# Optimization experiments

Hardware: AMD Instinct MI355X
Metric: run time of the kernel (lower is better)

## Reference

```python
import jax, jax.numpy as jnp
import numpy as np
import math

L, D_T, D, NL, NH, FFN, C, B = 24, 1024, 256, 12, 4, 1024, 2, 2048
HD = D // NH


def _layernorm(x, g, b, eps=1e-5):
    m = jnp.mean(x, axis=-1, keepdims=True)
    v = jnp.mean(jnp.square(x - m), axis=-1, keepdims=True)
    return (x - m) * jax.lax.rsqrt(v + eps) * g + b


def _rotate_half(x):
    x1, x2 = jnp.split(x, 2, axis=-1)
    return jnp.concatenate([-x2, x1], axis=-1)


def setup_inputs() -> dict:
    key = jax.random.key(0)
    ks = iter(jax.random.split(key, 64))
    n = lambda shape, s=0.02: jax.random.normal(next(ks), shape, dtype=jnp.float32) * s
    inp = {}
    inp['teacher_cls'] = jax.random.normal(next(ks), (B, L, D_T), dtype=jnp.float32)
    # input LN + projection
    inp['in_ln_g'] = jnp.ones((D_T,), jnp.float32); inp['in_ln_b'] = jnp.zeros((D_T,), jnp.float32)
    inp['proj_w'] = n((D, D_T)); inp['proj_b'] = jnp.zeros((D,), jnp.float32)
    # RoPE caches (buffers)
    inv_freq = 1.0 / (10000.0 ** (np.arange(0, D, 2, dtype=np.float32) / D))
    t = np.arange(L, dtype=np.float32)
    freqs = np.einsum('i,j->ij', t, inv_freq)
    emb = np.concatenate([freqs, freqs], axis=-1)
    inp['cos_cached'] = jnp.asarray(np.cos(emb)[None])  # [1,L,D]
    inp['sin_cached'] = jnp.asarray(np.sin(emb)[None])
    inp['pre_ln_g'] = jnp.ones((D,), jnp.float32); inp['pre_ln_b'] = jnp.zeros((D,), jnp.float32)
    # stacked transformer layer params [NL, ...]
    inp['l_ln1_g'] = jnp.ones((NL, D), jnp.float32); inp['l_ln1_b'] = jnp.zeros((NL, D), jnp.float32)
    inp['l_inw'] = n((NL, 3 * D, D)); inp['l_inb'] = jnp.zeros((NL, 3 * D), jnp.float32)
    inp['l_outw'] = n((NL, D, D)); inp['l_outb'] = jnp.zeros((NL, D), jnp.float32)
    inp['l_ln2_g'] = jnp.ones((NL, D), jnp.float32); inp['l_ln2_b'] = jnp.zeros((NL, D), jnp.float32)
    inp['l_w12'] = n((NL, 2 * FFN, D)); inp['l_b12'] = jnp.zeros((NL, 2 * FFN), jnp.float32)
    inp['l_w3'] = n((NL, D, FFN)); inp['l_b3'] = jnp.zeros((NL, D), jnp.float32)
    inp['post_ln_g'] = jnp.ones((D,), jnp.float32); inp['post_ln_b'] = jnp.zeros((D,), jnp.float32)
    # entropy gate
    inp['eg_w1'] = n((L, D, 8), 0.01); inp['eg_b1'] = jnp.zeros((L, 8), jnp.float32)
    inp['eg_w2'] = n((L, 8, 1), 0.01); inp['eg_b2'] = jnp.zeros((L, 1), jnp.float32)
    # per-position heads (stacked)
    inp['halt_w'] = n((L, D + 1)); inp['halt_b'] = jnp.full((L,), -4.0, jnp.float32)
    inp['cls_w'] = n((L, C, D)); inp['cls_b'] = jnp.zeros((L, C), jnp.float32)
    return inp


def _mha(x, inw, inb, outw, outb, mask):
    Bb, Ll, Dd = x.shape
    qkv = x @ inw.T + inb                              # [B,L,3D]
    q, k, v = jnp.split(qkv, 3, axis=-1)
    def heads(t):
        return t.reshape(Bb, Ll, NH, HD).transpose(0, 2, 1, 3)  # [B,H,L,hd]
    q, k, v = heads(q), heads(k), heads(v)
    scores = jnp.einsum('bhqd,bhkd->bhqk', q, k) / math.sqrt(HD)
    scores = jnp.where(mask, -jnp.inf, scores)
    attn = jax.nn.softmax(scores, axis=-1)
    o = jnp.einsum('bhqk,bhkd->bhqd', attn, v)
    o = o.transpose(0, 2, 1, 3).reshape(Bb, Ll, Dd)
    return o @ outw.T + outb


def reference(teacher_cls, in_ln_g, in_ln_b, proj_w, proj_b, cos_cached, sin_cached,
              pre_ln_g, pre_ln_b, l_ln1_g, l_ln1_b, l_inw, l_inb, l_outw, l_outb,
              l_ln2_g, l_ln2_b, l_w12, l_b12, l_w3, l_b3, post_ln_g, post_ln_b,
              eg_w1, eg_b1, eg_w2, eg_b2, halt_w, halt_b, cls_w, cls_b):
    x = _layernorm(teacher_cls, in_ln_g, in_ln_b)
    x = x @ proj_w.T + proj_b                          # [B,L,D]
    x = x * cos_cached + _rotate_half(x) * sin_cached  # RoPE
    z = _layernorm(x, pre_ln_g, pre_ln_b)
    mask = jnp.triu(jnp.ones((L, L), bool), 1)         # causal
    for i in range(NL):
        xn = _layernorm(z, l_ln1_g[i], l_ln1_b[i])
        z = z + _mha(xn, l_inw[i], l_inb[i], l_outw[i], l_outb[i], mask)
        xn = _layernorm(z, l_ln2_g[i], l_ln2_b[i])
        w12_out = xn @ l_w12[i].T + l_b12[i]           # [B,L,2*FFN]
        x1, x2 = jnp.split(w12_out, 2, axis=-1)
        hidden = jax.nn.silu(x1) * x2
        z = z + hidden @ l_w3[i].T + l_b3[i]
    z = _layernorm(z, post_ln_g, post_ln_b)
    # batched per-position classifier heads
    class_logits = jnp.einsum('bld,lcd->blc', z, cls_w) + cls_b   # [B,L,C]
    log_probs = jax.nn.log_softmax(class_logits, axis=-1)
    probs = jnp.exp(log_probs)
    probs_safe = jnp.clip(probs, 1e-10, 1.0)
    ent = -jnp.sum(probs_safe * jnp.log(probs_safe), axis=-1, keepdims=True)
    ent_norm = jnp.clip(ent / math.log(C), 0.0, 1.0)              # [B,L,1]
    # entropy gate
    h = jnp.tanh(jnp.einsum('bld,ldh->blh', z, eg_w1) + eg_b1)
    gate = jax.nn.sigmoid(jnp.einsum('blh,lho->blo', h, eg_w2) + eg_b2)
    gated = ent_norm * gate                                        # [B,L,1]
    # batched per-position halting heads
    combined = jnp.concatenate([z, gated], axis=-1)                # [B,L,D+1]
    halting_logits = jnp.einsum('bld,ld->bl', combined, halt_w) + halt_b
    return (halting_logits, class_logits, z)
```

## Files before the change

kernel.cpp:

```cpp
#include <hip/hip_runtime.h>
#include <hip/hip_bf16.h>
#include <math.h>

#define L_SEQ 24
#define DT 1024
#define DM 256
#define NLAYER 12
#define NHEAD 4
#define HDIM 64
#define FFND 1024
#define NCLS 2
#define NBATCH 2048
#define NTOK (NBATCH*L_SEQ)

typedef float f32x4 __attribute__((ext_vector_type(4)));
typedef __bf16 bf16x4 __attribute__((ext_vector_type(4)));
typedef __bf16 bf16x8 __attribute__((ext_vector_type(8)));

#define GLDS16(gp, lp) __builtin_amdgcn_global_load_lds((const __attribute__((address_space(1))) void*)(gp), (__attribute__((address_space(3))) void*)(lp), 16, 0, 0)
#define VMWAIT(N) asm volatile("s_waitcnt vmcnt(" #N ")" ::: "memory")
#define LGKM0()   asm volatile("s_waitcnt lgkmcnt(0)" ::: "memory")

__device__ inline float wred_sum(float v){
#pragma unroll
  for (int o = 32; o > 0; o >>= 1) v += __shfl_xor(v, o);
  return v;
}
__device__ inline float wred_max(float v){
#pragma unroll
  for (int o = 32; o > 0; o >>= 1) v = fmaxf(v, __shfl_xor(v, o));
  return v;
}

__device__ __forceinline__ void stage16x32(const __bf16* __restrict__ g, int ldk, int k0,
                                           __bf16* ldsbase, int lane, int rowbase){
  int r = rowbase + (lane >> 2);
  int cs = (lane & 3) ^ ((lane >> 3) & 3);
  GLDS16(g + (size_t)r*ldk + k0 + cs*8, ldsbase);
}
__device__ __forceinline__ bf16x8 frag32(const __bf16* tile, int row, int lane){
  int p = (lane >> 4) ^ ((row >> 1) & 3);
  return *(const bf16x8*)(tile + (row << 5) + (p << 3));
}

__device__ __forceinline__ int xcd_work(){
  int nwg = gridDim.x, bid = blockIdx.x;
  return (bid & 7) * (nwg >> 3) + (bid >> 3);
}

__global__ void cvt_bf16_kernel(const float* __restrict__ in, __bf16* __restrict__ out, int n4){
  int i = blockIdx.x * blockDim.x + threadIdx.x;
  int stride = gridDim.x * blockDim.x;
  for (; i < n4; i += stride){
    float4 v = ((const float4*)in)[i];
    bf16x4 o;
    o[0] = (__bf16)v.x; o[1] = (__bf16)v.y; o[2] = (__bf16)v.z; o[3] = (__bf16)v.w;
    ((bf16x4*)out)[i] = o;
  }
}

__global__ __launch_bounds__(256) void ln1024_kernel(
    const float* __restrict__ in, const float* __restrict__ g, const float* __restrict__ bb,
    __bf16* __restrict__ out){
  int row = blockIdx.x;
  int tid = threadIdx.x, wid = tid >> 6, lane = tid & 63;
  float4 x = ((const float4*)(in + (size_t)row*DT))[tid];
  float s = x.x + x.y + x.z + x.w;
  float q = x.x*x.x + x.y*x.y + x.z*x.z + x.w*x.w;
  s = wred_sum(s); q = wred_sum(q);
  __shared__ float red[8];
  if (lane == 0){ red[wid] = s; red[4+wid] = q; }
  __syncthreads();
  s = red[0]+red[1]+red[2]+red[3];
  q = red[4]+red[5]+red[6]+red[7];
  float mean = s * (1.f/DT);
  float rstd = rsqrtf(q*(1.f/DT) - mean*mean + 1e-5f);
  float4 gv = ((const float4*)g)[tid], bv = ((const float4*)bb)[tid];
  bf16x4 o;
  o[0] = (__bf16)((x.x-mean)*rstd*gv.x + bv.x);
  o[1] = (__bf16)((x.y-mean)*rstd*gv.y + bv.y);
  o[2] = (__bf16)((x.z-mean)*rstd*gv.z + bv.z);
  o[3] = (__bf16)((x.w-mean)*rstd*gv.w + bv.w);
  ((bf16x4*)(out + (size_t)row*DT))[tid] = o;
}

__global__ __launch_bounds__(256) void rope_preln_kernel(
    float* __restrict__ z, const float* __restrict__ cosc, const float* __restrict__ sinc,
    const float* __restrict__ g, const float* __restrict__ bb,
    const float* __restrict__ g1, const float* __restrict__ b1, __bf16* __restrict__ xnb){
  int row = blockIdx.x*4 + (threadIdx.x >> 6);
  int lane = threadIdx.x & 63;
  int l = row % L_SEQ;
  float4 x = ((const float4*)(z + (size_t)row*DM))[lane];
  float4 p;
  p.x = __shfl_xor(x.x, 32); p.y = __shfl_xor(x.y, 32);
  p.z = __shfl_xor(x.z, 32); p.w = __shfl_xor(x.w, 32);
  float sgn = (lane < 32) ? -1.f : 1.f;
  float4 c = ((const float4*)(cosc + l*DM))[lane];
  float4 sn = ((const float4*)(sinc + l*DM))[lane];
  float4 xr;
  xr.x = x.x*c.x + sgn*p.x*sn.x;
  xr.y = x.y*c.y + sgn*p.y*sn.y;
  xr.z = x.z*c.z + sgn*p.z*sn.z;
  xr.w = x.w*c.w + sgn*p.w*sn.w;
  float s = wred_sum(xr.x + xr.y + xr.z + xr.w);
  float q = wred_sum(xr.x*xr.x + xr.y*xr.y + xr.z*xr.z + xr.w*xr.w);
  float mean = s * (1.f/DM);
  float rstd = rsqrtf(q*(1.f/DM) - mean*mean + 1e-5f);
  float4 gv = ((const float4*)g)[lane], bv = ((const float4*)bb)[lane];
  float4 y;
  y.x = (xr.x-mean)*rstd*gv.x + bv.x;
  y.y = (xr.y-mean)*rstd*gv.y + bv.y;
  y.z = (xr.z-mean)*rstd*gv.z + bv.z;
  y.w = (xr.w-mean)*rstd*gv.w + bv.w;
  ((float4*)(z + (size_t)row*DM))[lane] = y;
  float s2 = wred_sum(y.x + y.y + y.z + y.w);
  float q2 = wred_sum(y.x*y.x + y.y*y.y + y.z*y.z + y.w*y.w);
  float mean2 = s2 * (1.f/DM);
  float rstd2 = rsqrtf(q2*(1.f/DM) - mean2*mean2 + 1e-5f);
  float4 g1v = ((const float4*)g1)[lane], b1v = ((const float4*)b1)[lane];
  bf16x4 o;
  o[0] = (__bf16)((y.x-mean2)*rstd2*g1v.x + b1v.x);
  o[1] = (__bf16)((y.y-mean2)*rstd2*g1v.y + b1v.y);
  o[2] = (__bf16)((y.z-mean2)*rstd2*g1v.z + b1v.z);
  o[3] = (__bf16)((y.w-mean2)*rstd2*g1v.w + b1v.w);
  ((bf16x4*)(xnb + (size_t)row*DM))[lane] = o;
}

template<int MODE, int K>
__global__ __launch_bounds__(256) void gemm128_kernel(
    const __bf16* __restrict__ A, const __bf16* __restrict__ W,
    const float* __restrict__ bias,
    float* __restrict__ Cf, __bf16* __restrict__ Cb,
    int N, int nt){
  __shared__ __align__(16) __bf16 As[2][128*32];
  __shared__ __align__(16) __bf16 Bs[2][128*32];
  int work = xcd_work();
  int bm = work / nt, bn = work % nt;
  int wid = threadIdx.x >> 6, lane = threadIdx.x & 63;
  int wr = wid >> 1, wc = wid & 1;
  int li = lane & 15, g4 = (lane >> 4) << 2;
  f32x4 acc[4][4] = {};
  const __bf16* ga = A + (size_t)bm*128*K;
  const __bf16* gb = W + (size_t)bn*128*K;
  const int NT = K/32;
  auto STAGE = [&](int b, int t){
    int k0 = t*32;
    stage16x32(ga, K, k0, &As[b][(wid*32)<<5],      lane, wid*32);
    stage16x32(ga, K, k0, &As[b][(wid*32+16)<<5],   lane, wid*32+16);
    stage16x32(gb, K, k0, &Bs[b][(wid*32)<<5],      lane, wid*32);
    stage16x32(gb, K, k0, &Bs[b][(wid*32+16)<<5],   lane, wid*32+16);
  };
  STAGE(0, 0);
  STAGE(1, 1);
  int cur = 0;
  for (int t = 0; t < NT; t++){
    if (t + 1 < NT) { VMWAIT(4); } else { VMWAIT(0); }
    __builtin_amdgcn_s_barrier();
    bf16x8 xf[4], wf[4];
#pragma unroll
    for (int mi = 0; mi < 4; mi++) xf[mi] = frag32(As[cur], wr*64 + mi*16 + li, lane);
#pragma unroll
    for (int ni = 0; ni < 4; ni++) wf[ni] = frag32(Bs[cur], wc*64 + ni*16 + li, lane);
    LGKM0();
    __builtin_amdgcn_sched_barrier(0);
    __builtin_amdgcn_s_barrier();
    if (t + 2 < NT) STAGE(cur, t+2);
    __builtin_amdgcn_s_setprio(1);
#pragma unroll
    for (int ni = 0; ni < 4; ni++)
#pragma unroll
      for (int mi = 0; mi < 4; mi++)
        acc[ni][mi] = __builtin_amdgcn_mfma_f32_16x16x32_bf16(wf[ni], xf[mi], acc[ni][mi], 0, 0, 0);
    __builtin_amdgcn_s_setprio(0);
    cur ^= 1;
  }
#pragma unroll
  for (int mi = 0; mi < 4; mi++){
    int m = bm*128 + wr*64 + mi*16 + li;
#pragma unroll
    for (int ni = 0; ni < 4; ni++){
      int n = bn*128 + wc*64 + ni*16 + g4;
      f32x4 bv = *(const f32x4*)(bias + n);
      f32x4 o = acc[ni][mi] + bv;
      if (MODE == 0){
        *(f32x4*)(Cf + (size_t)m*N + n) = o;
      } else {
        bf16x4 ob;
        ob[0] = (__bf16)o[0]; ob[1] = (__bf16)o[1]; ob[2] = (__bf16)o[2]; ob[3] = (__bf16)o[3];
        *(bf16x4*)(Cb + (size_t)m*N + n) = ob;
      }
    }
  }
}

__global__ __launch_bounds__(256) void gemm_glu_kernel(
    const __bf16* __restrict__ A, const __bf16* __restrict__ W12,
    const float* __restrict__ bias, __bf16* __restrict__ H){
  __shared__ __align__(16) __bf16 As[2][128*32];
  __shared__ __align__(16) __bf16 B1s[2][128*32];
  __shared__ __align__(16) __bf16 B2s[2][128*32];
  const int K = 256;
  int work = xcd_work();
  int bm = work >> 3, bn = work & 7;
  int wid = threadIdx.x >> 6, lane = threadIdx.x & 63;
  int wr = wid >> 1, wc = wid & 1;
  int li = lane & 15, g4 = (lane >> 4) << 2;
  f32x4 acc1[4][4] = {}, acc2[4][4] = {};
  const __bf16* ga  = A   + (size_t)bm*128*K;
  const __bf16* gb1 = W12 + (size_t)bn*128*K;
  const __bf16* gb2 = gb1 + (size_t)1024*K;
  auto STAGE = [&](int b, int t){
    int k0 = t*32;
    stage16x32(ga,  K, k0, &As[b][(wid*32)<<5],     lane, wid*32);
    stage16x32(ga,  K, k0, &As[b][(wid*32+16)<<5],  lane, wid*32+16);
    stage16x32(gb1, K, k0, &B1s[b][(wid*32)<<5],    lane, wid*32);
    stage16x32(gb1, K, k0, &B1s[b][(wid*32+16)<<5], lane, wid*32+16);
    stage16x32(gb2, K, k0, &B2s[b][(wid*32)<<5],    lane, wid*32);
    stage16x32(gb2, K, k0, &B2s[b][(wid*32+16)<<5], lane, wid*32+16);
  };
  STAGE(0, 0);
  STAGE(1, 1);
  int cur = 0;
  for (int t = 0; t < 8; t++){
    if (t + 1 < 8) { VMWAIT(6); } else { VMWAIT(0); }
    __builtin_amdgcn_s_barrier();
    bf16x8 xf[4], w1f[4], w2f[4];
#pragma unroll
    for (int mi = 0; mi < 4; mi++) xf[mi] = frag32(As[cur], wr*64 + mi*16 + li, lane);
#pragma unroll
    for (int ni = 0; ni < 4; ni++){
      w1f[ni] = frag32(B1s[cur], wc*64 + ni*16 + li, lane);
      w2f[ni] = frag32(B2s[cur], wc*64 + ni*16 + li, lane);
    }
    LGKM0();
    __builtin_amdgcn_sched_barrier(0);
    __builtin_amdgcn_s_barrier();
    if (t + 2 < 8) STAGE(cur, t+2);
    __builtin_amdgcn_s_setprio(1);
#pragma unroll
    for (int ni = 0; ni < 4; ni++)
#pragma unroll
      for (int mi = 0; mi < 4; mi++){
        acc1[ni][mi] = __builtin_amdgcn_mfma_f32_16x16x32_bf16(w1f[ni], xf[mi], acc1[ni][mi], 0, 0, 0);
        acc2[ni][mi] = __builtin_amdgcn_mfma_f32_16x16x32_bf16(w2f[ni], xf[mi], acc2[ni][mi], 0, 0, 0);
      }
    __builtin_amdgcn_s_setprio(0);
    cur ^= 1;
  }
#pragma unroll
  for (int mi = 0; mi < 4; mi++){
    int m = bm*128 + wr*64 + mi*16 + li;
#pragma unroll
    for (int ni = 0; ni < 4; ni++){
      int n = bn*128 + wc*64 + ni*16 + g4;
      f32x4 b1v = *(const f32x4*)(bias + n);
      f32x4 b2v = *(const f32x4*)(bias + 1024 + n);
      bf16x4 ob;
#pragma unroll
      for (int r = 0; r < 4; r++){
        float v1 = acc1[ni][mi][r] + b1v[r];
        float v2 = acc2[ni][mi][r] + b2v[r];
        float sig = 1.f/(1.f + __expf(-v1));
        ob[r] = (__bf16)(v1*sig*v2);
      }
      *(bf16x4*)(H + (size_t)m*FFND + n) = ob;
    }
  }
}

template<int K>
__global__ __launch_bounds__(256) void gemm_ln_kernel(
    const __bf16* __restrict__ A, const __bf16* __restrict__ W,
    const float* __restrict__ bias, float* __restrict__ z,
    const float* __restrict__ lng, const float* __restrict__ lnb,
    __bf16* __restrict__ outb, float* __restrict__ outf){
  __shared__ __align__(16) __bf16 As[2][64*32];
  __shared__ __align__(16) __bf16 Bs[2][256*32];
  __shared__ float redS[64][4], redQ[64][4];
  int bm = blockIdx.x;
  int wid = threadIdx.x >> 6, lane = threadIdx.x & 63;
  int li = lane & 15, g4 = (lane >> 4) << 2;
  f32x4 acc[4][4] = {};
  const __bf16* ga = A + (size_t)bm*64*K;
  const int NT = K/32;
  auto STAGE = [&](int b, int t){
    int k0 = t*32;
    stage16x32(ga, K, k0, &As[b][(wid*16)<<5], lane, wid*16);
#pragma unroll
    for (int j = 0; j < 4; j++)
      stage16x32(W, K, k0, &Bs[b][(wid*64 + j*16)<<5], lane, wid*64 + j*16);
  };
  STAGE(0, 0);
  STAGE(1, 1);
  int cur = 0;
  for (int t = 0; t < NT; t++){
    if (t + 1 < NT) { VMWAIT(5); } else { VMWAIT(0); }
    __builtin_amdgcn_s_barrier();
    bf16x8 xf[4], wf[4];
#pragma unroll
    for (int mi = 0; mi < 4; mi++) xf[mi] = frag32(As[cur], mi*16 + li, lane);
#pragma unroll
    for (int ni = 0; ni < 4; ni++) wf[ni] = frag32(Bs[cur], wid*64 + ni*16 + li, lane);
    LGKM0();
    __builtin_amdgcn_sched_barrier(0);
    __builtin_amdgcn_s_barrier();
    if (t + 2 < NT) STAGE(cur, t+2);
    __builtin_amdgcn_s_setprio(1);
#pragma unroll
    for (int ni = 0; ni < 4; ni++)
#pragma unroll
      for (int mi = 0; mi < 4; mi++)
        acc[ni][mi] = __builtin_amdgcn_mfma_f32_16x16x32_bf16(wf[ni], xf[mi], acc[ni][mi], 0, 0, 0);
    __builtin_amdgcn_s_setprio(0);
    cur ^= 1;
  }
  float sA[4] = {}, qA[4] = {};
#pragma unroll
  for (int mi = 0; mi < 4; mi++){
    int m = bm*64 + mi*16 + li;
#pragma unroll
    for (int ni = 0; ni < 4; ni++){
      int n = wid*64 + ni*16 + g4;
      f32x4 zv = *(const f32x4*)(z + (size_t)m*DM + n);
      f32x4 bv = *(const f32x4*)(bias + n);
      f32x4 v = acc[ni][mi] + bv + zv;
      acc[ni][mi] = v;
      *(f32x4*)(z + (size_t)m*DM + n) = v;
#pragma unroll
      for (int r = 0; r < 4; r++){ sA[mi] += v[r]; qA[mi] += v[r]*v[r]; }
    }
  }
  __syncthreads();
#pragma unroll
  for (int mi = 0; mi < 4; mi++){
    float s = sA[mi], q = qA[mi];
    s += __shfl_xor(s, 16); q += __shfl_xor(q, 16);
    s += __shfl_xor(s, 32); q += __shfl_xor(q, 32);
    if ((lane >> 4) == 0){ redS[mi*16 + li][wid] = s; redQ[mi*16 + li][wid] = q; }
  }
  __syncthreads();
#pragma unroll
  for (int mi = 0; mi < 4; mi++){
    int ml = mi*16 + li;
    float s = redS[ml][0] + redS[ml][1] + redS[ml][2] + redS[ml][3];
    float q = redQ[ml][0] + redQ[ml][1] + redQ[ml][2] + redQ[ml][3];
    float mean = s * (1.f/DM);
    float rstd = rsqrtf(q*(1.f/DM) - mean*mean + 1e-5f);
    int m = bm*64 + ml;
#pragma unroll
    for (int ni = 0; ni < 4; ni++){
      int n = wid*64 + ni*16 + g4;
      f32x4 gv = *(const f32x4*)(lng + n);
      f32x4 bv = *(const f32x4*)(lnb + n);
      if (outb){
        bf16x4 o;
#pragma unroll
        for (int r = 0; r < 4; r++) o[r] = (__bf16)((acc[ni][mi][r] - mean)*rstd*gv[r] + bv[r]);
        *(bf16x4*)(outb + (size_t)m*DM + n) = o;
      } else {
        f32x4 o;
#pragma unroll
        for (int r = 0; r < 4; r++) o[r] = (acc[ni][mi][r] - mean)*rstd*gv[r] + bv[r];
        *(f32x4*)(outf + (size_t)m*DM + n) = o;
      }
    }
  }
}

__global__ __launch_bounds__(256) void attn_kernel(const __bf16* __restrict__ qkv, __bf16* __restrict__ ob){
  int b = blockIdx.x;
  int h = threadIdx.x >> 6, lane = threadIdx.x & 63;
  __shared__ __align__(16) __bf16 Qs[NHEAD][L_SEQ][HDIM];
  __shared__ __align__(16) __bf16 Ks[NHEAD][L_SEQ][HDIM];
  __shared__ float Ps[NHEAD][L_SEQ][L_SEQ];
  const __bf16* base = qkv + (size_t)b*L_SEQ*768;
  float V[L_SEQ];
#pragma unroll
  for (int t = 0; t < L_SEQ; t++){
    int sw = lane ^ ((t & 7) << 3);
    Qs[h][t][sw] = base[t*768 + h*64 + lane];
    Ks[h][t][sw] = base[t*768 + 256 + h*64 + lane];
    V[t] = (float)base[t*768 + 512 + h*64 + lane];
  }
  __syncthreads();
  for (int p = lane; p < L_SEQ*L_SEQ; p += 64){
    int q = p / L_SEQ, k = p - q*L_SEQ;
    if (k <= q){
      int qx = (q & 7) << 3, kx = (k & 7) << 3;
      const __bf16* qr = Qs[h][q];
      const __bf16* kr = Ks[h][k];
      float s = 0.f;
#pragma unroll
      for (int d = 0; d < 64; d += 4){
        bf16x4 qa = *(const bf16x4*)(qr + (d ^ qx));
        bf16x4 ka = *(const bf16x4*)(kr + (d ^ kx));
        s += (float)qa[0]*(float)ka[0] + (float)qa[1]*(float)ka[1]
           + (float)qa[2]*(float)ka[2] + (float)qa[3]*(float)ka[3];
      }
      Ps[h][q][k] = s * 0.125f;
    }
  }
  __syncthreads();
  for (int q = 0; q < L_SEQ; q++){
    float v = (lane <= q) ? Ps[h][q][lane] : -1e30f;
    float mx = wred_max(v);
    float e = (lane <= q) ? __expf(v - mx) : 0.f;
    float sm = wred_sum(e);
    if (lane < L_SEQ) Ps[h][q][lane] = e / sm;
  }
  __syncthreads();
  for (int q = 0; q < L_SEQ; q++){
    float o = 0.f;
    for (int k = 0; k <= q; k++) o += Ps[h][q][k] * V[k];
    ob[((size_t)b*L_SEQ + q)*DM + h*64 + lane] = (__bf16)o;
  }
}

__global__ __launch_bounds__(256) void heads_kernel(
    const float* __restrict__ z,
    const float* __restrict__ cls_w, const float* __restrict__ cls_b,
    const float* __restrict__ eg_w1, const float* __restrict__ eg_b1,
    const float* __restrict__ eg_w2, const float* __restrict__ eg_b2,
    const float* __restrict__ halt_w, const float* __restrict__ halt_b,
    float* __restrict__ halt_out, float* __restrict__ cls_out){
  int m = blockIdx.x*4 + (threadIdx.x >> 6);
  int lane = threadIdx.x & 63;
  int l = m % L_SEQ;
  float4 zv = ((const float4*)(z + (size_t)m*DM))[lane];
  float4 w0 = ((const float4*)(cls_w + ((size_t)l*2 + 0)*DM))[lane];
  float4 w1 = ((const float4*)(cls_w + ((size_t)l*2 + 1)*DM))[lane];
  float c0 = wred_sum(zv.x*w0.x + zv.y*w0.y + zv.z*w0.z + zv.w*w0.w) + cls_b[l*2 + 0];
  float c1 = wred_sum(zv.x*w1.x + zv.y*w1.y + zv.z*w1.z + zv.w*w1.w) + cls_b[l*2 + 1];
  float mx = fmaxf(c0, c1);
  float e0 = __expf(c0 - mx), e1 = __expf(c1 - mx);
  float inv = 1.f/(e0 + e1);
  float p0 = fminf(fmaxf(e0*inv, 1e-10f), 1.f);
  float p1 = fminf(fmaxf(e1*inv, 1e-10f), 1.f);
  float ent = -(p0*__logf(p0) + p1*__logf(p1));
  float entn = fminf(fmaxf(ent * 1.44269504f, 0.f), 1.f);
  const float4* wg = (const float4*)(eg_w1 + ((size_t)l*DM + 4*lane)*8);
  float hacc[8] = {};
#pragma unroll
  for (int dd = 0; dd < 4; dd++){
    float zd = (dd==0) ? zv.x : (dd==1) ? zv.y : (dd==2) ? zv.z : zv.w;
    float4 a = wg[dd*2], b = wg[dd*2 + 1];
    hacc[0] += zd*a.x; hacc[1] += zd*a.y; hacc[2] += zd*a.z; hacc[3] += zd*a.w;
    hacc[4] += zd*b.x; hacc[5] += zd*b.y; hacc[6] += zd*b.z; hacc[7] += zd*b.w;
  }
  float gin = 0.f;
#pragma unroll
  for (int j = 0; j < 8; j++){
    float hj = wred_sum(hacc[j]);
    hj = tanhf(hj + eg_b1[l*8 + j]);
    gin += hj * eg_w2[l*8 + j];
  }
  gin += eg_b2[l];
  float gate = 1.f/(1.f + __expf(-gin));
  float gated = entn * gate;
  const float* hw = halt_w + (size_t)l*257;
  float hp = zv.x*hw[4*lane] + zv.y*hw[4*lane+1] + zv.z*hw[4*lane+2] + zv.w*hw[4*lane+3];
  float hl = wred_sum(hp) + gated*hw[256] + halt_b[l];
  if (lane == 0) halt_out[m] = hl;
  if (lane < 2) cls_out[(size_t)m*2 + lane] = lane ? c1 : c0;
}

extern "C" void kernel_launch(void* const* d_in, const int* in_sizes, int n_in,
                              void* d_out, int out_size, void* d_ws, size_t ws_size,
                              hipStream_t stream){
  const float* teacher = (const float*)d_in[0];
  const float* in_ln_g = (const float*)d_in[1];
  const float* in_ln_b = (const float*)d_in[2];
  const float* proj_w  = (const float*)d_in[3];
  const float* proj_b  = (const float*)d_in[4];
  const float* cosc    = (const float*)d_in[5];
  const float* sinc    = (const float*)d_in[6];
  const float* pre_g   = (const float*)d_in[7];
  const float* pre_b   = (const float*)d_in[8];
  const float* l_ln1_g = (const float*)d_in[9];
  const float* l_ln1_b = (const float*)d_in[10];
  const float* l_inw   = (const float*)d_in[11];
  const float* l_inb   = (const float*)d_in[12];
  const float* l_outw  = (const float*)d_in[13];
  const float* l_outb  = (const float*)d_in[14];
  const float* l_ln2_g = (const float*)d_in[15];
  const float* l_ln2_b = (const float*)d_in[16];
  const float* l_w12   = (const float*)d_in[17];
  const float* l_b12   = (const float*)d_in[18];
  const float* l_w3    = (const float*)d_in[19];
  const float* l_b3    = (const float*)d_in[20];
  const float* post_g  = (const float*)d_in[21];
  const float* post_b  = (const float*)d_in[22];
  const float* eg_w1   = (const float*)d_in[23];
  const float* eg_b1   = (const float*)d_in[24];
  const float* eg_w2   = (const float*)d_in[25];
  const float* eg_b2   = (const float*)d_in[26];
  const float* halt_w  = (const float*)d_in[27];
  const float* halt_b  = (const float*)d_in[28];
  const float* cls_w   = (const float*)d_in[29];
  const float* cls_b   = (const float*)d_in[30];

  float* out = (float*)d_out;
  float* halt_out = out;
  float* cls_out  = out + NTOK;
  float* z_out    = out + NTOK + (size_t)NTOK*NCLS;

  char* ws = (char*)d_ws;
  size_t off = 0;
  auto alloc = [&](size_t bytes){ void* p = ws + off; off += (bytes + 255) & ~(size_t)255; return p; };
  float*  zbuf = (float*) alloc((size_t)NTOK*DM*4);
  __bf16* xnb  = (__bf16*)alloc((size_t)NTOK*DM*2);
  __bf16* qkvb = (__bf16*)alloc((size_t)NTOK*768*2);
  __bf16* obuf = (__bf16*)alloc((size_t)NTOK*DM*2);
  __bf16* bigb = (__bf16*)alloc((size_t)NTOK*1024*2);
  __bf16* w_proj = (__bf16*)alloc((size_t)262144*2);
  __bf16* w_in   = (__bf16*)alloc((size_t)2359296*2);
  __bf16* w_out  = (__bf16*)alloc((size_t)786432*2);
  __bf16* w_12   = (__bf16*)alloc((size_t)6291456*2);
  __bf16* w_3    = (__bf16*)alloc((size_t)3145728*2);

  cvt_bf16_kernel<<<256, 256, 0, stream>>>(proj_w, w_proj, 262144/4);
  cvt_bf16_kernel<<<1024, 256, 0, stream>>>(l_inw, w_in, 2359296/4);
  cvt_bf16_kernel<<<512, 256, 0, stream>>>(l_outw, w_out, 786432/4);
  cvt_bf16_kernel<<<2048, 256, 0, stream>>>(l_w12, w_12, 6291456/4);
  cvt_bf16_kernel<<<1024, 256, 0, stream>>>(l_w3, w_3, 3145728/4);

  ln1024_kernel<<<NTOK, 256, 0, stream>>>(teacher, in_ln_g, in_ln_b, bigb);
  gemm128_kernel<0, 1024><<<384*2, 256, 0, stream>>>(bigb, w_proj, proj_b, zbuf, nullptr, 256, 2);
  rope_preln_kernel<<<NTOK/4, 256, 0, stream>>>(zbuf, cosc, sinc, pre_g, pre_b, l_ln1_g, l_ln1_b, xnb);

  for (int i = 0; i < NLAYER; i++){
    gemm128_kernel<1, 256><<<384*6, 256, 0, stream>>>(xnb, w_in + (size_t)i*768*256, l_inb + i*768, nullptr, qkvb, 768, 6);
    attn_kernel<<<NBATCH, 256, 0, stream>>>(qkvb, obuf);
    gemm_ln_kernel<256><<<NTOK/64, 256, 0, stream>>>(obuf, w_out + (size_t)i*256*256, l_outb + i*256,
                                                     zbuf, l_ln2_g + i*256, l_ln2_b + i*256, xnb, nullptr);
    gemm_glu_kernel<<<384*8, 256, 0, stream>>>(xnb, w_12 + (size_t)i*2048*256, l_b12 + i*2048, bigb);
    bool last = (i == NLAYER-1);
    gemm_ln_kernel<1024><<<NTOK/64, 256, 0, stream>>>(bigb, w_3 + (size_t)i*256*1024, l_b3 + i*256,
                                                      zbuf,
                                                      last ? post_g : l_ln1_g + (i+1)*256,
                                                      last ? post_b : l_ln1_b + (i+1)*256,
                                                      last ? nullptr : xnb,
                                                      last ? z_out : nullptr);
  }

  heads_kernel<<<NTOK/4, 256, 0, stream>>>(z_out, cls_w, cls_b, eg_w1, eg_b1, eg_w2, eg_b2,
                                           halt_w, halt_b, halt_out, cls_out);
}
```

Before: 4.093 ms.

## Enlarge GEMM tiles to 256x256 with 512-thread blocks across all matmuls

Every GEMM kernel (projection, QKV, out-proj+LN, GLU, FFN-down+LN) moves to 512-thread workgroups with larger output tiles: 256 rows by 256 columns, or by 128 for GLU. Half the waves now stage A and the other half stage B. Each block loads a larger slab of operands, so data reuse per byte loaded from global memory goes up and block count and launch overhead go down. The cost is more accumulator registers per thread and more LDS per block, which lowers occupancy, and only 192 blocks are launched for the LN-fused GEMMs, which may leave some compute units idle.

```diff
diff --git a/kernel.cpp b/kernel.cpp
--- a/kernel.cpp
+++ b/kernel.cpp
@@ -128,28 +128,31 @@
 }
 
 template<int MODE, int K>
-__global__ __launch_bounds__(256) void gemm128_kernel(
+__global__ __launch_bounds__(512) void gemm512_kernel(
     const __bf16* __restrict__ A, const __bf16* __restrict__ W,
     const float* __restrict__ bias,
     float* __restrict__ Cf, __bf16* __restrict__ Cb,
     int N, int nt){
-  __shared__ __align__(16) __bf16 As[2][128*32];
-  __shared__ __align__(16) __bf16 Bs[2][128*32];
+  __shared__ __align__(16) __bf16 As[2][256*32];
+  __shared__ __align__(16) __bf16 Bs[2][256*32];
   int work = xcd_work();
   int bm = work / nt, bn = work % nt;
   int wid = threadIdx.x >> 6, lane = threadIdx.x & 63;
   int wr = wid >> 1, wc = wid & 1;
   int li = lane & 15, g4 = (lane >> 4) << 2;
-  f32x4 acc[4][4] = {};
-  const __bf16* ga = A + (size_t)bm*128*K;
-  const __bf16* gb = W + (size_t)bn*128*K;
+  f32x4 acc[8][4] = {};
+  const __bf16* ga = A + (size_t)bm*256*K;
+  const __bf16* gb = W + (size_t)bn*256*K;
   const int NT = K/32;
   auto STAGE = [&](int b, int t){
     int k0 = t*32;
-    stage16x32(ga, K, k0, &As[b][(wid*32)<<5],      lane, wid*32);
-    stage16x32(ga, K, k0, &As[b][(wid*32+16)<<5],   lane, wid*32+16);
-    stage16x32(gb, K, k0, &Bs[b][(wid*32)<<5],      lane, wid*32);
-    stage16x32(gb, K, k0, &Bs[b][(wid*32+16)<<5],   lane, wid*32+16);
+    if (wid < 4){
+#pragma unroll
+      for (int j = 0; j < 4; j++){ int r = (wid*4 + j)*16; stage16x32(ga, K, k0, &As[b][r<<5], lane, r); }
+    } else {
+#pragma unroll
+      for (int j = 0; j < 4; j++){ int r = ((wid-4)*4 + j)*16; stage16x32(gb, K, k0, &Bs[b][r<<5], lane, r); }
+    }
   };
   STAGE(0, 0);
   STAGE(1, 1);
@@ -157,18 +160,18 @@
   for (int t = 0; t < NT; t++){
     if (t + 1 < NT) { VMWAIT(4); } else { VMWAIT(0); }
     __builtin_amdgcn_s_barrier();
-    bf16x8 xf[4], wf[4];
+    bf16x8 xf[4], wf[8];
 #pragma unroll
     for (int mi = 0; mi < 4; mi++) xf[mi] = frag32(As[cur], wr*64 + mi*16 + li, lane);
 #pragma unroll
-    for (int ni = 0; ni < 4; ni++) wf[ni] = frag32(Bs[cur], wc*64 + ni*16 + li, lane);
+    for (int ni = 0; ni < 8; ni++) wf[ni] = frag32(Bs[cur], wc*128 + ni*16 + li, lane);
     LGKM0();
     __builtin_amdgcn_sched_barrier(0);
     __builtin_amdgcn_s_barrier();
     if (t + 2 < NT) STAGE(cur, t+2);
     __builtin_amdgcn_s_setprio(1);
 #pragma unroll
-    for (int ni = 0; ni < 4; ni++)
+    for (int ni = 0; ni < 8; ni++)
 #pragma unroll
       for (int mi = 0; mi < 4; mi++)
         acc[ni][mi] = __builtin_amdgcn_mfma_f32_16x16x32_bf16(wf[ni], xf[mi], acc[ni][mi], 0, 0, 0);
@@ -177,10 +180,10 @@
   }
 #pragma unroll
   for (int mi = 0; mi < 4; mi++){
-    int m = bm*128 + wr*64 + mi*16 + li;
-#pragma unroll
-    for (int ni = 0; ni < 4; ni++){
-      int n = bn*128 + wc*64 + ni*16 + g4;
+    int m = bm*256 + wr*64 + mi*16 + li;
+#pragma unroll
+    for (int ni = 0; ni < 8; ni++){
+      int n = bn*256 + wc*128 + ni*16 + g4;
       f32x4 bv = *(const f32x4*)(bias + n);
       f32x4 o = acc[ni][mi] + bv;
       if (MODE == 0){
@@ -194,10 +197,10 @@
   }
 }
 
-__global__ __launch_bounds__(256) void gemm_glu_kernel(
+__global__ __launch_bounds__(512) void gemm_glu_kernel(
     const __bf16* __restrict__ A, const __bf16* __restrict__ W12,
     const float* __restrict__ bias, __bf16* __restrict__ H){
-  __shared__ __align__(16) __bf16 As[2][128*32];
+  __shared__ __align__(16) __bf16 As[2][256*32];
   __shared__ __align__(16) __bf16 B1s[2][128*32];
   __shared__ __align__(16) __bf16 B2s[2][128*32];
   const int K = 256;
@@ -207,23 +210,27 @@
   int wr = wid >> 1, wc = wid & 1;
   int li = lane & 15, g4 = (lane >> 4) << 2;
   f32x4 acc1[4][4] = {}, acc2[4][4] = {};
-  const __bf16* ga  = A   + (size_t)bm*128*K;
+  const __bf16* ga  = A   + (size_t)bm*256*K;
   const __bf16* gb1 = W12 + (size_t)bn*128*K;
   const __bf16* gb2 = gb1 + (size_t)1024*K;
   auto STAGE = [&](int b, int t){
     int k0 = t*32;
-    stage16x32(ga,  K, k0, &As[b][(wid*32)<<5],     lane, wid*32);
-    stage16x32(ga,  K, k0, &As[b][(wid*32+16)<<5],  lane, wid*32+16);
-    stage16x32(gb1, K, k0, &B1s[b][(wid*32)<<5],    lane, wid*32);
-    stage16x32(gb1, K, k0, &B1s[b][(wid*32+16)<<5], lane, wid*32+16);
-    stage16x32(gb2, K, k0, &B2s[b][(wid*32)<<5],    lane, wid*32);
-    stage16x32(gb2, K, k0, &B2s[b][(wid*32+16)<<5], lane, wid*32+16);
+    if (wid < 4){
+#pragma unroll
+      for (int j = 0; j < 4; j++){ int r = (wid*4 + j)*16; stage16x32(ga, K, k0, &As[b][r<<5], lane, r); }
+    } else if (wid < 6){
+#pragma unroll
+      for (int j = 0; j < 4; j++){ int r = ((wid-4)*4 + j)*16; stage16x32(gb1, K, k0, &B1s[b][r<<5], lane, r); }
+    } else {
+#pragma unroll
+      for (int j = 0; j < 4; j++){ int r = ((wid-6)*4 + j)*16; stage16x32(gb2, K, k0, &B2s[b][r<<5], lane, r); }
+    }
   };
   STAGE(0, 0);
   STAGE(1, 1);
   int cur = 0;
   for (int t = 0; t < 8; t++){
-    if (t + 1 < 8) { VMWAIT(6); } else { VMWAIT(0); }
+    if (t + 1 < 8) { VMWAIT(4); } else { VMWAIT(0); }
     __builtin_amdgcn_s_barrier();
     bf16x8 xf[4], w1f[4], w2f[4];
 #pragma unroll
@@ -250,7 +257,7 @@
   }
 #pragma unroll
   for (int mi = 0; mi < 4; mi++){
-    int m = bm*128 + wr*64 + mi*16 + li;
+    int m = bm*256 + wr*64 + mi*16 + li;
 #pragma unroll
     for (int ni = 0; ni < 4; ni++){
       int n = bn*128 + wc*64 + ni*16 + g4;
@@ -270,45 +277,49 @@
 }
 
 template<int K>
-__global__ __launch_bounds__(256) void gemm_ln_kernel(
+__global__ __launch_bounds__(512) void gemm_ln_kernel(
     const __bf16* __restrict__ A, const __bf16* __restrict__ W,
     const float* __restrict__ bias, float* __restrict__ z,
     const float* __restrict__ lng, const float* __restrict__ lnb,
     __bf16* __restrict__ outb, float* __restrict__ outf){
-  __shared__ __align__(16) __bf16 As[2][64*32];
+  __shared__ __align__(16) __bf16 As[2][256*32];
   __shared__ __align__(16) __bf16 Bs[2][256*32];
-  __shared__ float redS[64][4], redQ[64][4];
-  int bm = blockIdx.x;
+  __shared__ float redS[256][2], redQ[256][2];
+  int bm = xcd_work();
   int wid = threadIdx.x >> 6, lane = threadIdx.x & 63;
+  int wr = wid >> 1, wc = wid & 1;
   int li = lane & 15, g4 = (lane >> 4) << 2;
-  f32x4 acc[4][4] = {};
-  const __bf16* ga = A + (size_t)bm*64*K;
+  f32x4 acc[8][4] = {};
+  const __bf16* ga = A + (size_t)bm*256*K;
   const int NT = K/32;
   auto STAGE = [&](int b, int t){
     int k0 = t*32;
-    stage16x32(ga, K, k0, &As[b][(wid*16)<<5], lane, wid*16);
-#pragma unroll
-    for (int j = 0; j < 4; j++)
-      stage16x32(W, K, k0, &Bs[b][(wid*64 + j*16)<<5], lane, wid*64 + j*16);
+    if (wid < 4){
+#pragma unroll
+      for (int j = 0; j < 4; j++){ int r = (wid*4 + j)*16; stage16x32(ga, K, k0, &As[b][r<<5], lane, r); }
+    } else {
+#pragma unroll
+      for (int j = 0; j < 4; j++){ int r = ((wid-4)*4 + j)*16; stage16x32(W, K, k0, &Bs[b][r<<5], lane, r); }
+    }
   };
   STAGE(0, 0);
   STAGE(1, 1);
   int cur = 0;
   for (int t = 0; t < NT; t++){
-    if (t + 1 < NT) { VMWAIT(5); } else { VMWAIT(0); }
+    if (t + 1 < NT) { VMWAIT(4); } else { VMWAIT(0); }
     __builtin_amdgcn_s_barrier();
-    bf16x8 xf[4], wf[4];
-#pragma unroll
-    for (int mi = 0; mi < 4; mi++) xf[mi] = frag32(As[cur], mi*16 + li, lane);
-#pragma unroll
-    for (int ni = 0; ni < 4; ni++) wf[ni] = frag32(Bs[cur], wid*64 + ni*16 + li, lane);
+    bf16x8 xf[4], wf[8];
+#pragma unroll
+    for (int mi = 0; mi < 4; mi++) xf[mi] = frag32(As[cur], wr*64 + mi*16 + li, lane);
+#pragma unroll
+    for (int ni = 0; ni < 8; ni++) wf[ni] = frag32(Bs[cur], wc*128 + ni*16 + li, lane);
     LGKM0();
     __builtin_amdgcn_sched_barrier(0);
     __builtin_amdgcn_s_barrier();
     if (t + 2 < NT) STAGE(cur, t+2);
     __builtin_amdgcn_s_setprio(1);
 #pragma unroll
-    for (int ni = 0; ni < 4; ni++)
+    for (int ni = 0; ni < 8; ni++)
 #pragma unroll
       for (int mi = 0; mi < 4; mi++)
         acc[ni][mi] = __builtin_amdgcn_mfma_f32_16x16x32_bf16(wf[ni], xf[mi], acc[ni][mi], 0, 0, 0);
@@ -318,10 +329,10 @@
   float sA[4] = {}, qA[4] = {};
 #pragma unroll
   for (int mi = 0; mi < 4; mi++){
-    int m = bm*64 + mi*16 + li;
-#pragma unroll
-    for (int ni = 0; ni < 4; ni++){
-      int n = wid*64 + ni*16 + g4;
+    int m = bm*256 + wr*64 + mi*16 + li;
+#pragma unroll
+    for (int ni = 0; ni < 8; ni++){
+      int n = wc*128 + ni*16 + g4;
       f32x4 zv = *(const f32x4*)(z + (size_t)m*DM + n);
       f32x4 bv = *(const f32x4*)(bias + n);
       f32x4 v = acc[ni][mi] + bv + zv;
@@ -337,20 +348,20 @@
     float s = sA[mi], q = qA[mi];
     s += __shfl_xor(s, 16); q += __shfl_xor(q, 16);
     s += __shfl_xor(s, 32); q += __shfl_xor(q, 32);
-    if ((lane >> 4) == 0){ redS[mi*16 + li][wid] = s; redQ[mi*16 + li][wid] = q; }
+    if (lane < 16){ redS[wr*64 + mi*16 + li][wc] = s; redQ[wr*64 + mi*16 + li][wc] = q; }
   }
   __syncthreads();
 #pragma unroll
   for (int mi = 0; mi < 4; mi++){
-    int ml = mi*16 + li;
-    float s = redS[ml][0] + redS[ml][1] + redS[ml][2] + redS[ml][3];
-    float q = redQ[ml][0] + redQ[ml][1] + redQ[ml][2] + redQ[ml][3];
+    int ml = wr*64 + mi*16 + li;
+    float s = redS[ml][0] + redS[ml][1];
+    float q = redQ[ml][0] + redQ[ml][1];
     float mean = s * (1.f/DM);
     float rstd = rsqrtf(q*(1.f/DM) - mean*mean + 1e-5f);
-    int m = bm*64 + ml;
-#pragma unroll
-    for (int ni = 0; ni < 4; ni++){
-      int n = wid*64 + ni*16 + g4;
+    int m = bm*256 + ml;
+#pragma unroll
+    for (int ni = 0; ni < 8; ni++){
+      int n = wc*128 + ni*16 + g4;
       f32x4 gv = *(const f32x4*)(lng + n);
       f32x4 bv = *(const f32x4*)(lnb + n);
       if (outb){
@@ -526,22 +537,22 @@
   cvt_bf16_kernel<<<1024, 256, 0, stream>>>(l_w3, w_3, 3145728/4);
 
   ln1024_kernel<<<NTOK, 256, 0, stream>>>(teacher, in_ln_g, in_ln_b, bigb);
-  gemm128_kernel<0, 1024><<<384*2, 256, 0, stream>>>(bigb, w_proj, proj_b, zbuf, nullptr, 256, 2);
+  gemm512_kernel<0, 1024><<<192, 512, 0, stream>>>(bigb, w_proj, proj_b, zbuf, nullptr, 256, 1);
   rope_preln_kernel<<<NTOK/4, 256, 0, stream>>>(zbuf, cosc, sinc, pre_g, pre_b, l_ln1_g, l_ln1_b, xnb);
 
   for (int i = 0; i < NLAYER; i++){
-    gemm128_kernel<1, 256><<<384*6, 256, 0, stream>>>(xnb, w_in + (size_t)i*768*256, l_inb + i*768, nullptr, qkvb, 768, 6);
+    gemm512_kernel<1, 256><<<576, 512, 0, stream>>>(xnb, w_in + (size_t)i*768*256, l_inb + i*768, nullptr, qkvb, 768, 3);
     attn_kernel<<<NBATCH, 256, 0, stream>>>(qkvb, obuf);
-    gemm_ln_kernel<256><<<NTOK/64, 256, 0, stream>>>(obuf, w_out + (size_t)i*256*256, l_outb + i*256,
-                                                     zbuf, l_ln2_g + i*256, l_ln2_b + i*256, xnb, nullptr);
-    gemm_glu_kernel<<<384*8, 256, 0, stream>>>(xnb, w_12 + (size_t)i*2048*256, l_b12 + i*2048, bigb);
+    gemm_ln_kernel<256><<<192, 512, 0, stream>>>(obuf, w_out + (size_t)i*256*256, l_outb + i*256,
+                                                 zbuf, l_ln2_g + i*256, l_ln2_b + i*256, xnb, nullptr);
+    gemm_glu_kernel<<<1536, 512, 0, stream>>>(xnb, w_12 + (size_t)i*2048*256, l_b12 + i*2048, bigb);
     bool last = (i == NLAYER-1);
-    gemm_ln_kernel<1024><<<NTOK/64, 256, 0, stream>>>(bigb, w_3 + (size_t)i*256*1024, l_b3 + i*256,
-                                                      zbuf,
-                                                      last ? post_g : l_ln1_g + (i+1)*256,
-                                                      last ? post_b : l_ln1_b + (i+1)*256,
-                                                      last ? nullptr : xnb,
-                                                      last ? z_out : nullptr);
+    gemm_ln_kernel<1024><<<192, 512, 0, stream>>>(bigb, w_3 + (size_t)i*256*1024, l_b3 + i*256,
+                                                  zbuf,
+                                                  last ? post_g : l_ln1_g + (i+1)*256,
+                                                  last ? post_b : l_ln1_b + (i+1)*256,
+                                                  last ? nullptr : xnb,
+                                                  last ? z_out : nullptr);
   }
 
   heads_kernel<<<NTOK/4, 256, 0, stream>>>(z_out, cls_w, cls_b, eg_w1, eg_b1, eg_w2, eg_b2,
```

Result: faster. 3.942 ms (-3.7%).
